# Optimization experiments

Measured on AMD Instinct MI355X. Metric: run time of the kernel, lower is better.

## Reference

```python
import jax, jax.numpy as jnp
import numpy as np

N = 8192
TD, ID, D = 768, 1024, 1024
E = 8
GH = D // 2  # gate hidden
EPS = 1e-5


def _init_linear(key, fan_in, shape):
    # torch nn.Linear default init: U(-1/sqrt(fan_in), 1/sqrt(fan_in))
    bound = 1.0 / np.sqrt(fan_in)
    return jax.random.uniform(key, shape, jnp.float32, -bound, bound)


def setup_inputs() -> dict:
    key = jax.random.key(0)
    ks = jax.random.split(key, 16)
    return {
        "text_features": jax.random.normal(ks[0], (N, TD), jnp.float32),
        "image_features": jax.random.normal(ks[1], (N, ID), jnp.float32),
        "Wt": _init_linear(ks[2], TD, (TD, D)),
        "bt": _init_linear(ks[3], TD, (D,)),
        "Wi": _init_linear(ks[4], ID, (ID, D)),
        "bi": _init_linear(ks[5], ID, (D,)),
        "eW1": _init_linear(ks[6], 2 * D, (E, 2 * D, D)),
        "eb1": _init_linear(ks[7], 2 * D, (E, D)),
        "eW2": _init_linear(ks[8], D, (E, D, D)),
        "eb2": _init_linear(ks[9], D, (E, D)),
        "ln_g": jnp.ones((E, D), jnp.float32),
        "ln_b": jnp.zeros((E, D), jnp.float32),
        "gW1": _init_linear(ks[10], 2 * D, (2 * D, GH)),
        "gb1": _init_linear(ks[11], 2 * D, (GH,)),
        "gW2": _init_linear(ks[12], GH, (GH, E)),
        "gb2": _init_linear(ks[13], GH, (E,)),
    }


def reference(text_features, image_features, Wt, bt, Wi, bi,
              eW1, eb1, eW2, eb2, ln_g, ln_b, gW1, gb1, gW2, gb2):
    # project both modalities to shared dim D (dropout is identity in eval)
    ta = text_features @ Wt + bt            # [N, D]
    ia = image_features @ Wi + bi           # [N, D]
    c = jnp.concatenate([ta, ia], axis=-1)  # [N, 2D]

    # gating MLP -> softmax over experts
    gh = jax.nn.silu(c @ gW1 + gb1)                      # [N, GH]
    w = jax.nn.softmax(gh @ gW2 + gb2, axis=-1)          # [N, E]

    # all experts densely, batched over E
    h = jax.nn.silu(jnp.einsum('nc,ecd->ned', c, eW1) + eb1)   # [N, E, D]
    o = jnp.einsum('ned,edf->nef', h, eW2) + eb2               # [N, E, D]

    # per-expert LayerNorm over last dim
    mu = o.mean(axis=-1, keepdims=True)
    var = ((o - mu) ** 2).mean(axis=-1, keepdims=True)
    o = (o - mu) * jax.lax.rsqrt(var + EPS) * ln_g + ln_b      # [N, E, D]

    # gate-weighted sum over experts
    return jnp.einsum('ned,ne->nd', o, w)                      # [N, D]
```

## Files before the change

kernel.cpp:

```cpp
#include <hip/hip_runtime.h>

#define NROWS 8192
#define TDIM 768
#define IDIM 1024
#define DDIM 1024
#define NEXP 8
#define GHID 512

typedef __attribute__((ext_vector_type(8))) short short8;
typedef __attribute__((ext_vector_type(4))) float f4;
typedef __attribute__((ext_vector_type(4))) unsigned short us4;

__device__ __forceinline__ unsigned short f2bf(float f) {
  union { float f; unsigned u; } v; v.f = f;
  unsigned r = v.u + 0x7FFF + ((v.u >> 16) & 1);
  return (unsigned short)(r >> 16);
}
__device__ __forceinline__ float bf2f(unsigned short u) {
  union { unsigned u; float f; } v; v.u = ((unsigned)u) << 16;
  return v.f;
}

__device__ __forceinline__ void gload16(const void* g, void* l) {
  __builtin_amdgcn_global_load_lds(
      (const __attribute__((address_space(1))) void*)g,
      (__attribute__((address_space(3))) void*)l, 16, 0, 0);
}

__global__ __launch_bounds__(256) void cast_bf16_kernel(
    const float* __restrict__ src, unsigned short* __restrict__ dst, int n4) {
  int i = blockIdx.x * 256 + threadIdx.x;
  if (i < n4) {
    f4 v = ((const f4*)src)[i];
    us4 o;
    o[0] = f2bf(v[0]); o[1] = f2bf(v[1]); o[2] = f2bf(v[2]); o[3] = f2bf(v[3]);
    ((us4*)dst)[i] = o;
  }
}

__global__ __launch_bounds__(256) void transpose_cast_kernel(
    const float* __restrict__ src, unsigned short* __restrict__ dst, int R, int C) {
  __shared__ float tile[32][33];
  size_t base = (size_t)blockIdx.z * R * C;
  int c0 = blockIdx.x * 32, r0 = blockIdx.y * 32;
  int tx = threadIdx.x, ty = threadIdx.y;
#pragma unroll
  for (int j = 0; j < 32; j += 8)
    tile[ty + j][tx] = src[base + (size_t)(r0 + ty + j) * C + c0 + tx];
  __syncthreads();
#pragma unroll
  for (int j = 0; j < 32; j += 8)
    dst[base + (size_t)(c0 + ty + j) * R + r0 + tx] = f2bf(tile[tx][ty + j]);
}

template <int SILU, int OUTBF, int COLMAJ>
__global__ __launch_bounds__(512, 1) void gemm256_kernel(
    const unsigned short* __restrict__ A, const unsigned short* __restrict__ BT,
    const float* __restrict__ bias, void* __restrict__ Cptr,
    int K, int lda, int ldb, int ldc,
    size_t sA, size_t sB, size_t sBias, size_t sC) {
  __shared__ __align__(16) char LDS[131072];

  const unsigned short* Ab = A + (size_t)blockIdx.z * sA;
  const unsigned short* Bb = BT + (size_t)blockIdx.z * sB;
  const float* biasb = bias + (size_t)blockIdx.z * sBias;

  const int gx = gridDim.x, gy = gridDim.y;
  const int nwg = gx * gy;
  const int orig = blockIdx.y * gx + blockIdx.x;
  const int q = nwg >> 3, r = nwg & 7;
  const int xcd = orig & 7, idx = orig >> 3;
  const int wgid = (xcd < r ? xcd * (q + 1) : r * (q + 1) + (xcd - r) * q) + idx;
  const int bx = COLMAJ ? (wgid / gy) : (wgid % gx);
  const int by = COLMAJ ? (wgid % gy) : (wgid / gx);

  const int tid = threadIdx.x;
  const int wave = tid >> 6, lane = tid & 63;
  const int wm = wave >> 2, wn = wave & 3;
  const int row0 = by * 256, col0 = bx * 256;

  f4 acc[8][4] = {};

  const int srow = tid >> 3;
  const int scolg = ((tid & 7) << 4) ^ (((tid >> 3) & 7) << 4);
  const size_t lda2 = (size_t)lda * 2, ldb2 = (size_t)ldb * 2;
  const char* Abytes = (const char*)Ab;
  const char* Bbytes = (const char*)Bb;
  const size_t aG = (size_t)(row0 + srow) * lda2 + scolg;
  const size_t bG = (size_t)(col0 + srow) * ldb2 + scolg;
  char* ldsw = LDS + wave * 1024;

  auto stageA0 = [&](int tt) {
    const size_t kb = (size_t)tt << 7;
    char* d = ldsw + ((tt & 1) << 16);
    gload16(Abytes + aG + kb, d);
    gload16(Abytes + aG + (size_t)64 * lda2 + kb, d + 8192);
  };
  auto stageA1 = [&](int tt) {
    const size_t kb = (size_t)tt << 7;
    char* d = ldsw + ((tt & 1) << 16);
    gload16(Abytes + aG + (size_t)128 * lda2 + kb, d + 16384);
    gload16(Abytes + aG + (size_t)192 * lda2 + kb, d + 24576);
  };
  auto stageB0 = [&](int tt) {
    const size_t kb = (size_t)tt << 7;
    char* d = ldsw + ((tt & 1) << 16) + 32768;
    gload16(Bbytes + bG + kb, d);
    gload16(Bbytes + bG + (size_t)64 * ldb2 + kb, d + 8192);
  };
  auto stageB1 = [&](int tt) {
    const size_t kb = (size_t)tt << 7;
    char* d = ldsw + ((tt & 1) << 16) + 32768;
    gload16(Bbytes + bG + (size_t)128 * ldb2 + kb, d + 16384);
    gload16(Bbytes + bG + (size_t)192 * ldb2 + kb, d + 24576);
  };

  const int aBase = (wm * 128 + (lane & 15)) * 128;
  const int bBase = 32768 + (wn * 64 + (lane & 15)) * 128;
  const int ck0 = ((lane >> 4) << 4) ^ ((lane & 7) << 4);

  const int NT = K >> 6;

  stageA0(0); stageA1(0); stageB0(0); stageB1(0);
  if (NT > 1) { stageB0(1); stageB1(1); }
  asm volatile("s_waitcnt vmcnt(4)" ::: "memory");
  __builtin_amdgcn_s_barrier();

  short8 bv[4][2];
  for (int t = 0; t < NT; t++) {
    const int aB = ((t & 1) << 16) + aBase;
    const int bB = ((t & 1) << 16) + bBase;

    {
      short8 av[2][2];
#pragma unroll
      for (int n = 0; n < 4; n++)
#pragma unroll
        for (int kk = 0; kk < 2; kk++)
          bv[n][kk] = *(const short8*)(LDS + bB + n * 2048 + (ck0 ^ (kk << 6)));
#pragma unroll
      for (int m = 0; m < 2; m++)
#pragma unroll
        for (int kk = 0; kk < 2; kk++)
          av[m][kk] = *(const short8*)(LDS + aB + m * 2048 + (ck0 ^ (kk << 6)));
      if (t + 1 < NT) stageA0(t + 1);
      asm volatile("s_waitcnt lgkmcnt(8)" ::: "memory");
      __builtin_amdgcn_sched_barrier(0);
      __builtin_amdgcn_s_barrier();
      asm volatile("s_waitcnt lgkmcnt(0)" ::: "memory");
      __builtin_amdgcn_sched_barrier(0);
      __builtin_amdgcn_s_setprio(1);
#pragma unroll
      for (int kk = 0; kk < 2; kk++)
#pragma unroll
        for (int m = 0; m < 2; m++)
#pragma unroll
          for (int n = 0; n < 4; n++)
            acc[m][n] = __builtin_amdgcn_mfma_f32_16x16x32_bf16(av[m][kk], bv[n][kk], acc[m][n], 0, 0, 0);
      __builtin_amdgcn_s_setprio(0);
      __builtin_amdgcn_s_barrier();
    }

#pragma unroll
    for (int ph = 1; ph < 4; ph++) {
      short8 av[2][2];
#pragma unroll
      for (int m = 0; m < 2; m++)
#pragma unroll
        for (int kk = 0; kk < 2; kk++)
          av[m][kk] = *(const short8*)(LDS + aB + (ph * 2 + m) * 2048 + (ck0 ^ (kk << 6)));
      if (ph == 1) {
        if (t + 1 < NT) stageA1(t + 1);
        if (t + 2 < NT) stageB0(t + 2);
      } else if (ph == 2) {
        if (t + 2 < NT) stageB1(t + 2);
      }
      __builtin_amdgcn_sched_barrier(0);
      __builtin_amdgcn_s_barrier();
      asm volatile("s_waitcnt lgkmcnt(0)" ::: "memory");
      __builtin_amdgcn_sched_barrier(0);
      __builtin_amdgcn_s_setprio(1);
#pragma unroll
      for (int kk = 0; kk < 2; kk++)
#pragma unroll
        for (int m = 0; m < 2; m++)
#pragma unroll
          for (int n = 0; n < 4; n++)
            acc[ph * 2 + m][n] = __builtin_amdgcn_mfma_f32_16x16x32_bf16(av[m][kk], bv[n][kk], acc[ph * 2 + m][n], 0, 0, 0);
      __builtin_amdgcn_s_setprio(0);
      if (ph == 3) {
        if (t + 2 < NT) {
          asm volatile("s_waitcnt vmcnt(4)" ::: "memory");
        } else if (t + 1 < NT) {
          asm volatile("s_waitcnt vmcnt(0)" ::: "memory");
        }
      }
      __builtin_amdgcn_s_barrier();
    }
  }

  const int crow0 = row0 + wm * 128 + (lane >> 4) * 4;
  const int ccol0 = col0 + wn * 64 + (lane & 15);
  char* Cb = (char*)Cptr + (size_t)blockIdx.z * sC * (OUTBF ? 2 : 4);
#pragma unroll
  for (int n = 0; n < 4; n++) {
    const int col = ccol0 + n * 16;
    const float bvv = biasb[col];
#pragma unroll
    for (int m = 0; m < 8; m++) {
#pragma unroll
      for (int r2 = 0; r2 < 4; r2++) {
        float v = acc[m][n][r2] + bvv;
        if (SILU) v = v / (1.0f + __expf(-v));
        const size_t cidx = (size_t)(crow0 + m * 16 + r2) * ldc + col;
        if (OUTBF) ((unsigned short*)Cb)[cidx] = f2bf(v);
        else       ((float*)Cb)[cidx] = v;
      }
    }
  }
}

template <int SILU, int OUTBF>
__global__ __launch_bounds__(256) void gemm_tn_kernel(
    const unsigned short* __restrict__ A, const unsigned short* __restrict__ BT,
    const float* __restrict__ bias, void* __restrict__ Cptr,
    int K, int lda, int ldb, int ldc,
    size_t sA, size_t sB, size_t sBias, size_t sC) {
  __shared__ unsigned short Als[128 * 32];
  __shared__ unsigned short Bls[128 * 32];

  const unsigned short* Ab = A + (size_t)blockIdx.z * sA;
  const unsigned short* Bb = BT + (size_t)blockIdx.z * sB;
  const float* biasb = bias + (size_t)blockIdx.z * sBias;

  const int gx = gridDim.x;
  const int nwg = gx * gridDim.y;
  const int orig = blockIdx.y * gx + blockIdx.x;
  const int q = nwg >> 3, r = nwg & 7;
  const int xcd = orig & 7, idx = orig >> 3;
  const int wgid = (xcd < r ? xcd * (q + 1) : r * (q + 1) + (xcd - r) * q) + idx;
  const int bx = wgid % gx, by = wgid / gx;

  const int tid = threadIdx.x;
  const int wave = tid >> 6, lane = tid & 63;
  const int row0 = by * 128, col0 = bx * 128;
  const int wm = wave >> 1, wn = wave & 1;
  f4 acc[4][4] = {};

  const int aoff = (wm * 64 + (lane & 15)) * 32 + (lane >> 4) * 8;
  const int boff = (wn * 64 + (lane & 15)) * 32 + (lane >> 4) * 8;

  const int L0 = tid, L1 = tid + 256;
  const size_t aofs0 = (size_t)(row0 + (L0 >> 2)) * lda + (L0 & 3) * 8;
  const size_t aofs1 = (size_t)(row0 + (L1 >> 2)) * lda + (L1 & 3) * 8;
  const size_t bofs0 = (size_t)(col0 + (L0 >> 2)) * ldb + (L0 & 3) * 8;
  const size_t bofs1 = (size_t)(col0 + (L1 >> 2)) * ldb + (L1 & 3) * 8;
  char* abase0 = (char*)Als + wave * 1024;
  char* abase1 = (char*)Als + 4096 + wave * 1024;
  char* bbase0 = (char*)Bls + wave * 1024;
  char* bbase1 = (char*)Bls + 4096 + wave * 1024;

  for (int k0 = 0; k0 < K; k0 += 32) {
    gload16(Ab + aofs0 + k0, abase0);
    gload16(Ab + aofs1 + k0, abase1);
    gload16(Bb + bofs0 + k0, bbase0);
    gload16(Bb + bofs1 + k0, bbase1);
    __syncthreads();
    short8 af[4], bfr[4];
#pragma unroll
    for (int i = 0; i < 4; i++) af[i] = *(const short8*)&Als[aoff + i * 512];
#pragma unroll
    for (int j = 0; j < 4; j++) bfr[j] = *(const short8*)&Bls[boff + j * 512];
#pragma unroll
    for (int i = 0; i < 4; i++)
#pragma unroll
      for (int j = 0; j < 4; j++)
        acc[i][j] = __builtin_amdgcn_mfma_f32_16x16x32_bf16(af[i], bfr[j], acc[i][j], 0, 0, 0);
    __syncthreads();
  }

  const int crow = row0 + wm * 64 + (lane >> 4) * 4;
  const int ccol = col0 + wn * 64 + (lane & 15);
  char* Cb = (char*)Cptr + (size_t)blockIdx.z * sC * (OUTBF ? 2 : 4);
#pragma unroll
  for (int j = 0; j < 4; j++) {
    const int col = ccol + j * 16;
    const float bv = biasb[col];
#pragma unroll
    for (int i = 0; i < 4; i++) {
#pragma unroll
      for (int r2 = 0; r2 < 4; r2++) {
        float v = acc[i][j][r2] + bv;
        if (SILU) v = v / (1.0f + __expf(-v));
        const size_t cidx = (size_t)(crow + i * 16 + r2) * ldc + col;
        if (OUTBF)
          ((unsigned short*)Cb)[cidx] = f2bf(v);
        else
          ((float*)Cb)[cidx] = v;
      }
    }
  }
}

__global__ __launch_bounds__(256) void gate_kernel(
    const unsigned short* __restrict__ gh, const float* __restrict__ gW2,
    const float* __restrict__ gb2, float* __restrict__ wout) {
  __shared__ float sW[NEXP * GHID];
  int tid = threadIdx.x;
  for (int i = tid; i < GHID * NEXP; i += 256) {
    int k = i >> 3, e = i & 7;
    sW[e * GHID + k] = gW2[i];
  }
  __syncthreads();
  int wave = tid >> 6, lane = tid & 63;
  int row = blockIdx.x * 4 + wave;
  float acc[NEXP] = {};
#pragma unroll
  for (int i = 0; i < 8; i++) {
    int k = lane + 64 * i;
    float x = bf2f(gh[(size_t)row * GHID + k]);
#pragma unroll
    for (int e = 0; e < NEXP; e++) acc[e] += x * sW[e * GHID + k];
  }
#pragma unroll
  for (int off = 32; off; off >>= 1)
#pragma unroll
    for (int e = 0; e < NEXP; e++) acc[e] += __shfl_xor(acc[e], off);
  float lg[NEXP], mx = -1e30f;
#pragma unroll
  for (int e = 0; e < NEXP; e++) { lg[e] = acc[e] + gb2[e]; mx = fmaxf(mx, lg[e]); }
  float s = 0.f;
#pragma unroll
  for (int e = 0; e < NEXP; e++) { lg[e] = __expf(lg[e] - mx); s += lg[e]; }
  if (lane < NEXP) wout[(size_t)row * NEXP + lane] = lg[lane] / s;
}

__global__ __launch_bounds__(256) void ln_acc8_kernel(
    const unsigned short* __restrict__ o, const float* __restrict__ wgate,
    const float* __restrict__ ln_g, const float* __restrict__ ln_b,
    float* __restrict__ out, int row0) {
  int wave = threadIdx.x >> 6, lane = threadIdx.x & 63;
  int lrow = blockIdx.x * 4 + wave;
  int grow = row0 + lrow;
  float res[16];
#pragma unroll
  for (int u = 0; u < 16; u++) res[u] = 0.f;
#pragma unroll
  for (int e = 0; e < NEXP; e++) {
    const unsigned short* orow = o + (size_t)lrow * (NEXP * DDIM) + (size_t)e * DDIM;
    float xs[16];
    float s = 0.f, s2 = 0.f;
#pragma unroll
    for (int qq = 0; qq < 2; qq++) {
      short8 t = *(const short8*)&orow[qq * 512 + lane * 8];
#pragma unroll
      for (int u = 0; u < 8; u++) {
        float x = bf2f((unsigned short)t[u]);
        xs[qq * 8 + u] = x;
        s += x;
        s2 += x * x;
      }
    }
#pragma unroll
    for (int off = 32; off; off >>= 1) {
      s += __shfl_xor(s, off);
      s2 += __shfl_xor(s2, off);
    }
    const float inv = 1.0f / 1024.0f;
    float mu = s * inv;
    float var = s2 * inv - mu * mu;
    float rr = rsqrtf(var + 1e-5f);
    float wv = wgate[(size_t)grow * NEXP + e];
#pragma unroll
    for (int qq = 0; qq < 2; qq++) {
      int d = qq * 512 + lane * 8;
#pragma unroll
      for (int u = 0; u < 8; u++) {
        float gg = ln_g[(size_t)e * DDIM + d + u];
        float bb = ln_b[(size_t)e * DDIM + d + u];
        res[qq * 8 + u] += wv * ((xs[qq * 8 + u] - mu) * rr * gg + bb);
      }
    }
  }
  size_t rowbase = (size_t)grow * DDIM;
#pragma unroll
  for (int qq = 0; qq < 2; qq++) {
#pragma unroll
    for (int h = 0; h < 2; h++) {
      f4 t;
#pragma unroll
      for (int u = 0; u < 4; u++) t[u] = res[qq * 8 + h * 4 + u];
      *(f4*)&out[rowbase + qq * 512 + lane * 8 + h * 4] = t;
    }
  }
}

extern "C" void kernel_launch(void* const* d_in, const int* in_sizes, int n_in,
                              void* d_out, int out_size, void* d_ws, size_t ws_size,
                              hipStream_t stream) {
  const float* text  = (const float*)d_in[0];
  const float* image = (const float*)d_in[1];
  const float* Wt    = (const float*)d_in[2];
  const float* bt    = (const float*)d_in[3];
  const float* Wi    = (const float*)d_in[4];
  const float* bi    = (const float*)d_in[5];
  const float* eW1   = (const float*)d_in[6];
  const float* eb1   = (const float*)d_in[7];
  const float* eW2   = (const float*)d_in[8];
  const float* eb2   = (const float*)d_in[9];
  const float* ln_g  = (const float*)d_in[10];
  const float* ln_b  = (const float*)d_in[11];
  const float* gW1   = (const float*)d_in[12];
  const float* gb1   = (const float*)d_in[13];
  const float* gW2   = (const float*)d_in[14];
  const float* gb2   = (const float*)d_in[15];
  float* out = (float*)d_out;

  size_t off = 0;
  auto alloc = [&](size_t bytes) -> void* {
    void* p = (char*)d_ws + off;
    off += (bytes + 255) & ~(size_t)255;
    return p;
  };
  unsigned short* eW1T = (unsigned short*)alloc((size_t)NEXP * 2 * DDIM * DDIM * 2);
  unsigned short* eW2T = (unsigned short*)alloc((size_t)NEXP * DDIM * DDIM * 2);
  unsigned short* c_bf = (unsigned short*)alloc((size_t)NROWS * 2 * DDIM * 2);
  float* wgate         = (float*)alloc((size_t)NROWS * NEXP * 4);
  const size_t overlay0 = off;

  unsigned short* text_bf = (unsigned short*)alloc((size_t)NROWS * TDIM * 2);
  unsigned short* img_bf  = (unsigned short*)alloc((size_t)NROWS * IDIM * 2);
  unsigned short* WtT     = (unsigned short*)alloc((size_t)TDIM * DDIM * 2);
  unsigned short* WiT     = (unsigned short*)alloc((size_t)IDIM * DDIM * 2);
  unsigned short* gW1T    = (unsigned short*)alloc((size_t)2 * DDIM * GHID * 2);
  unsigned short* gh_bf   = (unsigned short*)alloc((size_t)NROWS * GHID * 2);

  int slab = 8192;
  while (slab > 256 &&
         overlay0 + (size_t)slab * (size_t)(2 * NEXP * DDIM + 2 * NEXP * DDIM) > ws_size)
    slab >>= 1;
  unsigned short* h_slab = (unsigned short*)((char*)d_ws + overlay0);
  unsigned short* o_slab = (unsigned short*)((char*)d_ws + overlay0 +
                                             (size_t)slab * NEXP * DDIM * 2);

  cast_bf16_kernel<<<(NROWS * TDIM / 4 + 255) / 256, 256, 0, stream>>>(text, text_bf, NROWS * TDIM / 4);
  cast_bf16_kernel<<<(NROWS * IDIM / 4 + 255) / 256, 256, 0, stream>>>(image, img_bf, NROWS * IDIM / 4);

  transpose_cast_kernel<<<dim3(DDIM / 32, TDIM / 32, 1), dim3(32, 8), 0, stream>>>(Wt, WtT, TDIM, DDIM);
  transpose_cast_kernel<<<dim3(DDIM / 32, IDIM / 32, 1), dim3(32, 8), 0, stream>>>(Wi, WiT, IDIM, DDIM);
  transpose_cast_kernel<<<dim3(GHID / 32, 2 * DDIM / 32, 1), dim3(32, 8), 0, stream>>>(gW1, gW1T, 2 * DDIM, GHID);
  transpose_cast_kernel<<<dim3(DDIM / 32, 2 * DDIM / 32, NEXP), dim3(32, 8), 0, stream>>>(eW1, eW1T, 2 * DDIM, DDIM);
  transpose_cast_kernel<<<dim3(DDIM / 32, DDIM / 32, NEXP), dim3(32, 8), 0, stream>>>(eW2, eW2T, DDIM, DDIM);

  gemm_tn_kernel<0, 1><<<dim3(DDIM / 128, NROWS / 128), 256, 0, stream>>>(
      text_bf, WtT, bt, c_bf, TDIM, TDIM, TDIM, 2 * DDIM, 0, 0, 0, 0);
  gemm_tn_kernel<0, 1><<<dim3(DDIM / 128, NROWS / 128), 256, 0, stream>>>(
      img_bf, WiT, bi, c_bf + DDIM, IDIM, IDIM, IDIM, 2 * DDIM, 0, 0, 0, 0);

  gemm_tn_kernel<1, 1><<<dim3(GHID / 128, NROWS / 128), 256, 0, stream>>>(
      c_bf, gW1T, gb1, gh_bf, 2 * DDIM, 2 * DDIM, 2 * DDIM, GHID, 0, 0, 0, 0);

  gate_kernel<<<NROWS / 4, 256, 0, stream>>>(gh_bf, gW2, gb2, wgate);

  for (int r0 = 0; r0 < NROWS; r0 += slab) {
    gemm256_kernel<1, 1, 1><<<dim3(NEXP * DDIM / 256, slab / 256), 512, 0, stream>>>(
        c_bf + (size_t)r0 * 2 * DDIM, eW1T, eb1, h_slab,
        2 * DDIM, 2 * DDIM, 2 * DDIM, NEXP * DDIM, 0, 0, 0, 0);
    gemm256_kernel<0, 1, 0><<<dim3(DDIM / 256, slab / 256, NEXP), 512, 0, stream>>>(
        h_slab, eW2T, eb2, o_slab,
        DDIM, NEXP * DDIM, DDIM, NEXP * DDIM,
        (size_t)DDIM, (size_t)DDIM * DDIM, (size_t)DDIM, (size_t)DDIM);
    ln_acc8_kernel<<<slab / 4, 256, 0, stream>>>(o_slab, wgate, ln_g, ln_b, out, r0);
  }
}
```

Before: 702.0 us.

## Widen transpose tiles, merge projection GEMMs, respread B prefetch stages

The weight transpose-cast kernel now uses 64x64 tiles and writes eight bf16 values per 16-byte vector store, replacing scalar 2-byte stores. The two modality projection GEMMs become a single launch with a z dimension that selects text or image, which removes one launch and lets the two run together. In the 256-tile expert GEMM, the B-tile prefetches for the next stage are spread across phases 2 and 3 instead of being issued together. The new projection kernel is a simple non-pipelined, single-buffered loop that may be slower per tile than the old gemm_tn kernel, and its column-strided transpose reads from LDS may cause bank conflicts.

After: 698.3 us. No clear change (-0.5%).

```diff
diff --git a/kernel.cpp b/kernel.cpp
--- a/kernel.cpp
+++ b/kernel.cpp
@@ -40,17 +40,24 @@
 
 __global__ __launch_bounds__(256) void transpose_cast_kernel(
     const float* __restrict__ src, unsigned short* __restrict__ dst, int R, int C) {
-  __shared__ float tile[32][33];
+  __shared__ float tile[64][65];
   size_t base = (size_t)blockIdx.z * R * C;
-  int c0 = blockIdx.x * 32, r0 = blockIdx.y * 32;
-  int tx = threadIdx.x, ty = threadIdx.y;
-#pragma unroll
-  for (int j = 0; j < 32; j += 8)
+  int c0 = blockIdx.x * 64, r0 = blockIdx.y * 64;
+  int tx = threadIdx.x & 63, ty = threadIdx.x >> 6;
+#pragma unroll
+  for (int j = 0; j < 64; j += 4)
     tile[ty + j][tx] = src[base + (size_t)(r0 + ty + j) * C + c0 + tx];
   __syncthreads();
-#pragma unroll
-  for (int j = 0; j < 32; j += 8)
-    dst[base + (size_t)(c0 + ty + j) * R + r0 + tx] = f2bf(tile[tx][ty + j]);
+  const int tid = threadIdx.x;
+#pragma unroll
+  for (int i = 0; i < 2; i++) {
+    int row = i * 32 + (tid >> 3);
+    int c8 = (tid & 7) * 8;
+    short8 v;
+#pragma unroll
+    for (int u = 0; u < 8; u++) v[u] = (short)f2bf(tile[c8 + u][row]);
+    *(short8*)&dst[base + (size_t)(c0 + row) * R + r0 + c8] = v;
+  }
 }
 
 template <int SILU, int OUTBF, int COLMAJ>
@@ -171,8 +178,9 @@
           av[m][kk] = *(const short8*)(LDS + aB + (ph * 2 + m) * 2048 + (ck0 ^ (kk << 6)));
       if (ph == 1) {
         if (t + 1 < NT) stageA1(t + 1);
+      } else if (ph == 2) {
         if (t + 2 < NT) stageB0(t + 2);
-      } else if (ph == 2) {
+      } else {
         if (t + 2 < NT) stageB1(t + 2);
       }
       __builtin_amdgcn_sched_barrier(0);
@@ -297,6 +305,84 @@
           ((unsigned short*)Cb)[cidx] = f2bf(v);
         else
           ((float*)Cb)[cidx] = v;
+      }
+    }
+  }
+}
+
+__global__ __launch_bounds__(256) void proj2_kernel(
+    const unsigned short* __restrict__ A0, const unsigned short* __restrict__ A1,
+    const unsigned short* __restrict__ B0, const unsigned short* __restrict__ B1,
+    const float* __restrict__ bias0, const float* __restrict__ bias1,
+    unsigned short* __restrict__ Cptr) {
+  __shared__ unsigned short Als[128 * 32];
+  __shared__ unsigned short Bls[128 * 32];
+
+  const int z = blockIdx.z;
+  const unsigned short* Ab = z ? A1 : A0;
+  const unsigned short* Bb = z ? B1 : B0;
+  const float* biasb = z ? bias1 : bias0;
+  const int K = z ? IDIM : TDIM;
+  const int ldc = 2 * DDIM;
+
+  const int gx = gridDim.x;
+  const int nwg = gx * gridDim.y;
+  const int orig = blockIdx.y * gx + blockIdx.x;
+  const int q = nwg >> 3, r = nwg & 7;
+  const int xcd = orig & 7, idx = orig >> 3;
+  const int wgid = (xcd < r ? xcd * (q + 1) : r * (q + 1) + (xcd - r) * q) + idx;
+  const int bx = wgid % gx, by = wgid / gx;
+
+  const int tid = threadIdx.x;
+  const int wave = tid >> 6, lane = tid & 63;
+  const int row0 = by * 128, col0 = bx * 128;
+  const int wm = wave >> 1, wn = wave & 1;
+  f4 acc[4][4] = {};
+
+  const int aoff = (wm * 64 + (lane & 15)) * 32 + (lane >> 4) * 8;
+  const int boff = (wn * 64 + (lane & 15)) * 32 + (lane >> 4) * 8;
+
+  const int L0 = tid, L1 = tid + 256;
+  const size_t aofs0 = (size_t)(row0 + (L0 >> 2)) * K + (L0 & 3) * 8;
+  const size_t aofs1 = (size_t)(row0 + (L1 >> 2)) * K + (L1 & 3) * 8;
+  const size_t bofs0 = (size_t)(col0 + (L0 >> 2)) * K + (L0 & 3) * 8;
+  const size_t bofs1 = (size_t)(col0 + (L1 >> 2)) * K + (L1 & 3) * 8;
+  char* abase0 = (char*)Als + wave * 1024;
+  char* abase1 = (char*)Als + 4096 + wave * 1024;
+  char* bbase0 = (char*)Bls + wave * 1024;
+  char* bbase1 = (char*)Bls + 4096 + wave * 1024;
+
+  for (int k0 = 0; k0 < K; k0 += 32) {
+    gload16(Ab + aofs0 + k0, abase0);
+    gload16(Ab + aofs1 + k0, abase1);
+    gload16(Bb + bofs0 + k0, bbase0);
+    gload16(Bb + bofs1 + k0, bbase1);
+    __syncthreads();
+    short8 af[4], bfr[4];
+#pragma unroll
+    for (int i = 0; i < 4; i++) af[i] = *(const short8*)&Als[aoff + i * 512];
+#pragma unroll
+    for (int j = 0; j < 4; j++) bfr[j] = *(const short8*)&Bls[boff + j * 512];
+#pragma unroll
+    for (int i = 0; i < 4; i++)
+#pragma unroll
+      for (int j = 0; j < 4; j++)
+        acc[i][j] = __builtin_amdgcn_mfma_f32_16x16x32_bf16(af[i], bfr[j], acc[i][j], 0, 0, 0);
+    __syncthreads();
+  }
+
+  const int crow = row0 + wm * 64 + (lane >> 4) * 4;
+  const int ccol = z * DDIM + col0 + wn * 64 + (lane & 15);
+#pragma unroll
+  for (int j = 0; j < 4; j++) {
+    const int col = ccol + j * 16;
+    const float bv = biasb[col0 + wn * 64 + (lane & 15) + j * 16];
+#pragma unroll
+    for (int i = 0; i < 4; i++) {
+#pragma unroll
+      for (int r2 = 0; r2 < 4; r2++) {
+        float v = acc[i][j][r2] + bv;
+        Cptr[(size_t)(crow + i * 16 + r2) * ldc + col] = f2bf(v);
       }
     }
   }
@@ -446,16 +532,14 @@
   cast_bf16_kernel<<<(NROWS * TDIM / 4 + 255) / 256, 256, 0, stream>>>(text, text_bf, NROWS * TDIM / 4);
   cast_bf16_kernel<<<(NROWS * IDIM / 4 + 255) / 256, 256, 0, stream>>>(image, img_bf, NROWS * IDIM / 4);
 
-  transpose_cast_kernel<<<dim3(DDIM / 32, TDIM / 32, 1), dim3(32, 8), 0, stream>>>(Wt, WtT, TDIM, DDIM);
-  transpose_cast_kernel<<<dim3(DDIM / 32, IDIM / 32, 1), dim3(32, 8), 0, stream>>>(Wi, WiT, IDIM, DDIM);
-  transpose_cast_kernel<<<dim3(GHID / 32, 2 * DDIM / 32, 1), dim3(32, 8), 0, stream>>>(gW1, gW1T, 2 * DDIM, GHID);
-  transpose_cast_kernel<<<dim3(DDIM / 32, 2 * DDIM / 32, NEXP), dim3(32, 8), 0, stream>>>(eW1, eW1T, 2 * DDIM, DDIM);
-  transpose_cast_kernel<<<dim3(DDIM / 32, DDIM / 32, NEXP), dim3(32, 8), 0, stream>>>(eW2, eW2T, DDIM, DDIM);
-
-  gemm_tn_kernel<0, 1><<<dim3(DDIM / 128, NROWS / 128), 256, 0, stream>>>(
-      text_bf, WtT, bt, c_bf, TDIM, TDIM, TDIM, 2 * DDIM, 0, 0, 0, 0);
-  gemm_tn_kernel<0, 1><<<dim3(DDIM / 128, NROWS / 128), 256, 0, stream>>>(
-      img_bf, WiT, bi, c_bf + DDIM, IDIM, IDIM, IDIM, 2 * DDIM, 0, 0, 0, 0);
+  transpose_cast_kernel<<<dim3(DDIM / 64, TDIM / 64, 1), 256, 0, stream>>>(Wt, WtT, TDIM, DDIM);
+  transpose_cast_kernel<<<dim3(DDIM / 64, IDIM / 64, 1), 256, 0, stream>>>(Wi, WiT, IDIM, DDIM);
+  transpose_cast_kernel<<<dim3(GHID / 64, 2 * DDIM / 64, 1), 256, 0, stream>>>(gW1, gW1T, 2 * DDIM, GHID);
+  transpose_cast_kernel<<<dim3(DDIM / 64, 2 * DDIM / 64, NEXP), 256, 0, stream>>>(eW1, eW1T, 2 * DDIM, DDIM);
+  transpose_cast_kernel<<<dim3(DDIM / 64, DDIM / 64, NEXP), 256, 0, stream>>>(eW2, eW2T, DDIM, DDIM);
+
+  proj2_kernel<<<dim3(DDIM / 128, NROWS / 128, 2), 256, 0, stream>>>(
+      text_bf, img_bf, WtT, WiT, bt, bi, c_bf);
 
   gemm_tn_kernel<1, 1><<<dim3(GHID / 128, NROWS / 128), 256, 0, stream>>>(
       c_bf, gW1T, gb1, gh_bf, 2 * DDIM, 2 * DDIM, 2 * DDIM, GHID, 0, 0, 0, 0);
```

## Batch modality projections into one padded GEMM and tune transpose, staging, epilogue

Applied to the files above, without the earlier changes.

The text and image projections are merged into one batched gemm256 launch. Text activations and weights are zero-padded to K=1024, and the two biases are copied into one buffer. The transpose-cast kernel moves to 64x64 tiles with vectorized 16-byte stores, and the expert-2 GEMM gets a z-major XCD-aware block mapping. The B-tile prefetch is spread across phases 1-3, and the epilogues are reordered to store row-contiguous columns. Padding adds wasted MACs on the text projection plus extra memset/copy traffic.

Result: faster. 651.4 us (-7.2%).

```diff
diff --git a/kernel.cpp b/kernel.cpp
--- a/kernel.cpp
+++ b/kernel.cpp
@@ -38,22 +38,44 @@
   }
 }
 
+__global__ __launch_bounds__(256) void cast_pad_kernel(
+    const float* __restrict__ src, unsigned short* __restrict__ dst, int n4) {
+  int i = blockIdx.x * 256 + threadIdx.x;
+  if (i < n4) {
+    f4 v = ((const f4*)src)[i];
+    us4 o;
+    o[0] = f2bf(v[0]); o[1] = f2bf(v[1]); o[2] = f2bf(v[2]); o[3] = f2bf(v[3]);
+    const int row = i / (TDIM / 4);
+    const int col4 = (i % (TDIM / 4)) * 4;
+    *(us4*)&dst[(size_t)row * 1024 + col4] = o;
+  }
+}
+
 __global__ __launch_bounds__(256) void transpose_cast_kernel(
-    const float* __restrict__ src, unsigned short* __restrict__ dst, int R, int C) {
-  __shared__ float tile[32][33];
-  size_t base = (size_t)blockIdx.z * R * C;
-  int c0 = blockIdx.x * 32, r0 = blockIdx.y * 32;
-  int tx = threadIdx.x, ty = threadIdx.y;
-#pragma unroll
-  for (int j = 0; j < 32; j += 8)
-    tile[ty + j][tx] = src[base + (size_t)(r0 + ty + j) * C + c0 + tx];
+    const float* __restrict__ src, unsigned short* __restrict__ dst, int R, int C,
+    int ldDst) {
+  __shared__ float tile[64][65];
+  size_t sbase = (size_t)blockIdx.z * R * C;
+  size_t dbase = (size_t)blockIdx.z * C * ldDst;
+  int c0 = blockIdx.x * 64, r0 = blockIdx.y * 64;
+  int tx = threadIdx.x & 63, ty = threadIdx.x >> 6;
+#pragma unroll
+  for (int j = 0; j < 64; j += 4)
+    tile[ty + j][tx] = src[sbase + (size_t)(r0 + ty + j) * C + c0 + tx];
   __syncthreads();
-#pragma unroll
-  for (int j = 0; j < 32; j += 8)
-    dst[base + (size_t)(c0 + ty + j) * R + r0 + tx] = f2bf(tile[tx][ty + j]);
-}
-
-template <int SILU, int OUTBF, int COLMAJ>
+  const int tid = threadIdx.x;
+#pragma unroll
+  for (int i = 0; i < 2; i++) {
+    int row = i * 32 + (tid >> 3);
+    int c8 = (tid & 7) * 8;
+    short8 v;
+#pragma unroll
+    for (int u = 0; u < 8; u++) v[u] = (short)f2bf(tile[c8 + u][row]);
+    *(short8*)&dst[dbase + (size_t)(c0 + row) * ldDst + r0 + c8] = v;
+  }
+}
+
+template <int SILU, int OUTBF, int COLMAJ, int ZXCD>
 __global__ __launch_bounds__(512, 1) void gemm256_kernel(
     const unsigned short* __restrict__ A, const unsigned short* __restrict__ BT,
     const float* __restrict__ bias, void* __restrict__ Cptr,
@@ -61,18 +83,28 @@
     size_t sA, size_t sB, size_t sBias, size_t sC) {
   __shared__ __align__(16) char LDS[131072];
 
-  const unsigned short* Ab = A + (size_t)blockIdx.z * sA;
-  const unsigned short* Bb = BT + (size_t)blockIdx.z * sB;
-  const float* biasb = bias + (size_t)blockIdx.z * sBias;
-
   const int gx = gridDim.x, gy = gridDim.y;
-  const int nwg = gx * gy;
-  const int orig = blockIdx.y * gx + blockIdx.x;
-  const int q = nwg >> 3, r = nwg & 7;
-  const int xcd = orig & 7, idx = orig >> 3;
-  const int wgid = (xcd < r ? xcd * (q + 1) : r * (q + 1) + (xcd - r) * q) + idx;
-  const int bx = COLMAJ ? (wgid / gy) : (wgid % gx);
-  const int by = COLMAJ ? (wgid % gy) : (wgid / gx);
+  int zz, bx, by;
+  if (ZXCD) {
+    const int lin = (blockIdx.z * gy + blockIdx.y) * gx + blockIdx.x;
+    zz = lin & 7;
+    const int rest = lin >> 3;
+    bx = rest % gx;
+    by = rest / gx;
+  } else {
+    zz = blockIdx.z;
+    const int nwg = gx * gy;
+    const int orig = blockIdx.y * gx + blockIdx.x;
+    const int q = nwg >> 3, r = nwg & 7;
+    const int xcd = orig & 7, idx = orig >> 3;
+    const int wgid = (xcd < r ? xcd * (q + 1) : r * (q + 1) + (xcd - r) * q) + idx;
+    bx = COLMAJ ? (wgid / gy) : (wgid % gx);
+    by = COLMAJ ? (wgid % gy) : (wgid / gx);
+  }
+
+  const unsigned short* Ab = A + (size_t)zz * sA;
+  const unsigned short* Bb = BT + (size_t)zz * sB;
+  const float* biasb = bias + (size_t)zz * sBias;
 
   const int tid = threadIdx.x;
   const int wave = tid >> 6, lane = tid & 63;
@@ -171,8 +203,9 @@
           av[m][kk] = *(const short8*)(LDS + aB + (ph * 2 + m) * 2048 + (ck0 ^ (kk << 6)));
       if (ph == 1) {
         if (t + 1 < NT) stageA1(t + 1);
+      } else if (ph == 2) {
         if (t + 2 < NT) stageB0(t + 2);
-      } else if (ph == 2) {
+      } else {
         if (t + 2 < NT) stageB1(t + 2);
       }
       __builtin_amdgcn_sched_barrier(0);
@@ -201,18 +234,20 @@
 
   const int crow0 = row0 + wm * 128 + (lane >> 4) * 4;
   const int ccol0 = col0 + wn * 64 + (lane & 15);
-  char* Cb = (char*)Cptr + (size_t)blockIdx.z * sC * (OUTBF ? 2 : 4);
-#pragma unroll
-  for (int n = 0; n < 4; n++) {
-    const int col = ccol0 + n * 16;
-    const float bvv = biasb[col];
-#pragma unroll
-    for (int m = 0; m < 8; m++) {
-#pragma unroll
-      for (int r2 = 0; r2 < 4; r2++) {
-        float v = acc[m][n][r2] + bvv;
+  char* Cb = (char*)Cptr + (size_t)zz * sC * (OUTBF ? 2 : 4);
+  float bvv[4];
+#pragma unroll
+  for (int n = 0; n < 4; n++) bvv[n] = biasb[ccol0 + n * 16];
+#pragma unroll
+  for (int m = 0; m < 8; m++) {
+#pragma unroll
+    for (int r2 = 0; r2 < 4; r2++) {
+      const size_t rowb = (size_t)(crow0 + m * 16 + r2) * ldc;
+#pragma unroll
+      for (int n = 0; n < 4; n++) {
+        float v = acc[m][n][r2] + bvv[n];
         if (SILU) v = v / (1.0f + __expf(-v));
-        const size_t cidx = (size_t)(crow0 + m * 16 + r2) * ldc + col;
+        const size_t cidx = rowb + ccol0 + n * 16;
         if (OUTBF) ((unsigned short*)Cb)[cidx] = f2bf(v);
         else       ((float*)Cb)[cidx] = v;
       }
@@ -282,17 +317,19 @@
   const int crow = row0 + wm * 64 + (lane >> 4) * 4;
   const int ccol = col0 + wn * 64 + (lane & 15);
   char* Cb = (char*)Cptr + (size_t)blockIdx.z * sC * (OUTBF ? 2 : 4);
-#pragma unroll
-  for (int j = 0; j < 4; j++) {
-    const int col = ccol + j * 16;
-    const float bv = biasb[col];
-#pragma unroll
-    for (int i = 0; i < 4; i++) {
-#pragma unroll
-      for (int r2 = 0; r2 < 4; r2++) {
-        float v = acc[i][j][r2] + bv;
+  float bvv[4];
+#pragma unroll
+  for (int j = 0; j < 4; j++) bvv[j] = biasb[ccol + j * 16];
+#pragma unroll
+  for (int i = 0; i < 4; i++) {
+#pragma unroll
+    for (int r2 = 0; r2 < 4; r2++) {
+      const size_t rowb = (size_t)(crow + i * 16 + r2) * ldc;
+#pragma unroll
+      for (int j = 0; j < 4; j++) {
+        float v = acc[i][j][r2] + bvv[j];
         if (SILU) v = v / (1.0f + __expf(-v));
-        const size_t cidx = (size_t)(crow + i * 16 + r2) * ldc + col;
+        const size_t cidx = rowb + ccol + j * 16;
         if (OUTBF)
           ((unsigned short*)Cb)[cidx] = f2bf(v);
         else
@@ -428,10 +465,9 @@
   float* wgate         = (float*)alloc((size_t)NROWS * NEXP * 4);
   const size_t overlay0 = off;
 
-  unsigned short* text_bf = (unsigned short*)alloc((size_t)NROWS * TDIM * 2);
-  unsigned short* img_bf  = (unsigned short*)alloc((size_t)NROWS * IDIM * 2);
-  unsigned short* WtT     = (unsigned short*)alloc((size_t)TDIM * DDIM * 2);
-  unsigned short* WiT     = (unsigned short*)alloc((size_t)IDIM * DDIM * 2);
+  unsigned short* act_pad = (unsigned short*)alloc((size_t)2 * NROWS * 1024 * 2);
+  unsigned short* wT_pad  = (unsigned short*)alloc((size_t)2 * 1024 * 1024 * 2);
+  float* bias2            = (float*)alloc((size_t)2 * 1024 * 4);
   unsigned short* gW1T    = (unsigned short*)alloc((size_t)2 * DDIM * GHID * 2);
   unsigned short* gh_bf   = (unsigned short*)alloc((size_t)NROWS * GHID * 2);
 
@@ -443,19 +479,31 @@
   unsigned short* o_slab = (unsigned short*)((char*)d_ws + overlay0 +
                                              (size_t)slab * NEXP * DDIM * 2);
 
-  cast_bf16_kernel<<<(NROWS * TDIM / 4 + 255) / 256, 256, 0, stream>>>(text, text_bf, NROWS * TDIM / 4);
-  cast_bf16_kernel<<<(NROWS * IDIM / 4 + 255) / 256, 256, 0, stream>>>(image, img_bf, NROWS * IDIM / 4);
-
-  transpose_cast_kernel<<<dim3(DDIM / 32, TDIM / 32, 1), dim3(32, 8), 0, stream>>>(Wt, WtT, TDIM, DDIM);
-  transpose_cast_kernel<<<dim3(DDIM / 32, IDIM / 32, 1), dim3(32, 8), 0, stream>>>(Wi, WiT, IDIM, DDIM);
-  transpose_cast_kernel<<<dim3(GHID / 32, 2 * DDIM / 32, 1), dim3(32, 8), 0, stream>>>(gW1, gW1T, 2 * DDIM, GHID);
-  transpose_cast_kernel<<<dim3(DDIM / 32, 2 * DDIM / 32, NEXP), dim3(32, 8), 0, stream>>>(eW1, eW1T, 2 * DDIM, DDIM);
-  transpose_cast_kernel<<<dim3(DDIM / 32, DDIM / 32, NEXP), dim3(32, 8), 0, stream>>>(eW2, eW2T, DDIM, DDIM);
-
-  gemm_tn_kernel<0, 1><<<dim3(DDIM / 128, NROWS / 128), 256, 0, stream>>>(
-      text_bf, WtT, bt, c_bf, TDIM, TDIM, TDIM, 2 * DDIM, 0, 0, 0, 0);
-  gemm_tn_kernel<0, 1><<<dim3(DDIM / 128, NROWS / 128), 256, 0, stream>>>(
-      img_bf, WiT, bi, c_bf + DDIM, IDIM, IDIM, IDIM, 2 * DDIM, 0, 0, 0, 0);
+  hipMemsetAsync(act_pad, 0, (size_t)NROWS * 1024 * 2, stream);
+  hipMemsetAsync(wT_pad, 0, (size_t)1024 * 1024 * 2, stream);
+  hipMemcpyAsync(bias2, bt, 1024 * sizeof(float), hipMemcpyDeviceToDevice, stream);
+  hipMemcpyAsync(bias2 + 1024, bi, 1024 * sizeof(float), hipMemcpyDeviceToDevice, stream);
+
+  cast_pad_kernel<<<(NROWS * TDIM / 4 + 255) / 256, 256, 0, stream>>>(
+      text, act_pad, NROWS * TDIM / 4);
+  cast_bf16_kernel<<<(NROWS * IDIM / 4 + 255) / 256, 256, 0, stream>>>(
+      image, act_pad + (size_t)NROWS * 1024, NROWS * IDIM / 4);
+
+  transpose_cast_kernel<<<dim3(DDIM / 64, TDIM / 64, 1), 256, 0, stream>>>(
+      Wt, wT_pad, TDIM, DDIM, 1024);
+  transpose_cast_kernel<<<dim3(DDIM / 64, IDIM / 64, 1), 256, 0, stream>>>(
+      Wi, wT_pad + (size_t)1024 * 1024, IDIM, DDIM, 1024);
+  transpose_cast_kernel<<<dim3(GHID / 64, 2 * DDIM / 64, 1), 256, 0, stream>>>(
+      gW1, gW1T, 2 * DDIM, GHID, 2 * DDIM);
+  transpose_cast_kernel<<<dim3(DDIM / 64, 2 * DDIM / 64, NEXP), 256, 0, stream>>>(
+      eW1, eW1T, 2 * DDIM, DDIM, 2 * DDIM);
+  transpose_cast_kernel<<<dim3(DDIM / 64, DDIM / 64, NEXP), 256, 0, stream>>>(
+      eW2, eW2T, DDIM, DDIM, DDIM);
+
+  gemm256_kernel<0, 1, 0, 0><<<dim3(DDIM / 256, NROWS / 256, 2), 512, 0, stream>>>(
+      act_pad, wT_pad, bias2, c_bf,
+      1024, 1024, 1024, 2 * DDIM,
+      (size_t)NROWS * 1024, (size_t)1024 * 1024, (size_t)1024, (size_t)DDIM);
 
   gemm_tn_kernel<1, 1><<<dim3(GHID / 128, NROWS / 128), 256, 0, stream>>>(
       c_bf, gW1T, gb1, gh_bf, 2 * DDIM, 2 * DDIM, 2 * DDIM, GHID, 0, 0, 0, 0);
@@ -463,10 +511,10 @@
   gate_kernel<<<NROWS / 4, 256, 0, stream>>>(gh_bf, gW2, gb2, wgate);
 
   for (int r0 = 0; r0 < NROWS; r0 += slab) {
-    gemm256_kernel<1, 1, 1><<<dim3(NEXP * DDIM / 256, slab / 256), 512, 0, stream>>>(
+    gemm256_kernel<1, 1, 1, 0><<<dim3(NEXP * DDIM / 256, slab / 256), 512, 0, stream>>>(
         c_bf + (size_t)r0 * 2 * DDIM, eW1T, eb1, h_slab,
         2 * DDIM, 2 * DDIM, 2 * DDIM, NEXP * DDIM, 0, 0, 0, 0);
-    gemm256_kernel<0, 1, 0><<<dim3(DDIM / 256, slab / 256, NEXP), 512, 0, stream>>>(
+    gemm256_kernel<0, 1, 0, 1><<<dim3(DDIM / 256, slab / 256, NEXP), 512, 0, stream>>>(
         h_slab, eW2T, eb2, o_slab,
         DDIM, NEXP * DDIM, DDIM, NEXP * DDIM,
         (size_t)DDIM, (size_t)DDIM * DDIM, (size_t)DDIM, (size_t)DDIM);
```
